# Performance work log

Hardware: AMD Instinct MI355X
Metric: run time of the kernel (lower is better)

## Reference

```python
import jax, jax.numpy as jnp
import numpy as np

H = 1024           # hidden_dim
BS = 32            # batch size
STEPS = 128        # number of chart steps
AMB = 32           # ambiguous decompositions per cell (padded fixed)
START = 256        # start_index: number of pre-filled leaf entries
CHART_LEN = START + STEPS


def setup_inputs() -> dict:
    key = jax.random.key(0)
    k1, k2, k3, k4 = jax.random.split(key, 4)
    chart = jax.random.normal(k1, (BS, CHART_LEN, 2 * H), dtype=jnp.float32)
    # (l, r) child positions per step/batch/ambiguity; valid filled entries in [0, START)
    operations = jax.random.randint(k2, (STEPS, BS, AMB, 2), 0, START, dtype=jnp.int32)
    U = jax.random.uniform(k3, (5 * H, 2 * H), dtype=jnp.float32)
    b = jnp.zeros((5 * H,), dtype=jnp.float32)
    energy_u = jax.random.uniform(k4, (H,), dtype=jnp.float32)
    return {"chart": chart, "operations": operations, "start_index": START,
            "U": U, "b": b, "energy_u": energy_u}


def reference(chart, operations, start_index, U, b, energy_u):
    h_dim = energy_u.shape[0]
    bs, amb = chart.shape[0], operations.shape[2]
    batch_idx = jnp.arange(bs)[:, None, None]  # [bs,1,1] for gather broadcast
    temperature = jnp.float32(1.0)
    eps = jnp.float32(1e-8)  # torch cosine_similarity eps
    u_norm = jnp.maximum(jnp.linalg.norm(energy_u), eps)

    def step_fn(ch, inp):
        step, ops = inp  # ops: [bs, amb, 2]
        # gather child chart entries: [bs, amb, 2, 2H]
        entries = ch[batch_idx, ops, :]
        ccL = entries[:, :, 0, :h_dim]                 # left cell state  [bs,amb,H]
        ccR = entries[:, :, 1, :h_dim]                 # right cell state [bs,amb,H]
        hh = entries[:, :, :, h_dim:].reshape(bs, amb, 2 * h_dim)  # [hL;hR]
        preact = jnp.einsum('bah,gh->bag', hh, U) + b  # [bs,amb,5H]
        i  = jax.nn.sigmoid(preact[..., :h_dim])
        fL = jax.nn.sigmoid(preact[..., h_dim:2 * h_dim])
        fR = jax.nn.sigmoid(preact[..., 2 * h_dim:3 * h_dim])
        o  = jax.nn.sigmoid(preact[..., 3 * h_dim:4 * h_dim])
        u  = jnp.tanh(preact[..., 4 * h_dim:])
        c = fL * ccL + fR * ccR + i * u                # [bs,amb,H]
        h = o * jnp.tanh(c)                            # [bs,amb,H]
        # cosine-similarity energy against learned vector energy_u
        h_norm = jnp.maximum(jnp.linalg.norm(h, axis=2), eps)  # [bs,amb]
        e = (h @ energy_u) / (u_norm * h_norm)                 # [bs,amb]
        s = jax.nn.softmax(e / temperature, axis=1)[..., None] # [bs,amb,1]
        combined = jnp.concatenate([(s * c).sum(axis=1), (s * h).sum(axis=1)], axis=-1)
        ch = ch.at[:, start_index + step, :].set(combined)
        return ch, None

    n_steps = operations.shape[0]
    chart, _ = jax.lax.scan(step_fn, chart, (jnp.arange(n_steps), operations))
    return chart
```

## Files before the change

### kernel.cpp

```cpp
#include <hip/hip_runtime.h>
#include <hip/hip_fp16.h>


typedef unsigned int u32;
typedef unsigned short u16;
typedef __attribute__((ext_vector_type(8))) short short8;
typedef __attribute__((ext_vector_type(4))) float f32x4;
typedef __attribute__((ext_vector_type(4))) u16 u16x4;
typedef _Float16 h8 __attribute__((ext_vector_type(8)));
typedef _Float16 h2v __attribute__((ext_vector_type(2)));
typedef _Float16 h4v __attribute__((ext_vector_type(4)));

#define CHART_ROWS 384
#define L2E 1.4426950408889634f

__device__ __forceinline__ u16 f2bf(float f) {
  u32 u = __float_as_uint(f);
  u32 r = u + 0x7fffu + ((u >> 16) & 1u);
  return (u16)(r >> 16);
}

__device__ __forceinline__ h2v pk_exp2(h2v x) {
  __half2 t = *(__half2*)&x;
  t = h2exp2(t);
  return *(h2v*)&t;
}
__device__ __forceinline__ h2v pk_rcp(h2v x) {
  __half2 t = *(__half2*)&x;
  t = h2rcp(t);
  return *(h2v*)&t;
}

#if __has_builtin(__builtin_amdgcn_fdot2)
__device__ __forceinline__ float fdot2a(h2v a, h2v b, float c) {
  return __builtin_amdgcn_fdot2(a, b, c, false);
}
#else
__device__ __forceinline__ float fdot2a(h2v a, h2v b, float c) {
  return c + (float)a[0] * (float)b[0] + (float)a[1] * (float)b[1];
}
#endif

__device__ __forceinline__ void async16(const void* g, void* l) {
  __builtin_amdgcn_global_load_lds((const __attribute__((address_space(1))) u32*)g,
                                   (__attribute__((address_space(3))) u32*)l, 16, 0, 0);
}

#define BAR() __builtin_amdgcn_s_barrier()
#define VMCNT4 asm volatile("s_waitcnt vmcnt(4)" ::: "memory")
#define VMCNT0 asm volatile("s_waitcnt vmcnt(0)" ::: "memory")

__global__ void k_cvt(const f32x4* __restrict__ U4, u16* __restrict__ Ubf,
                      const float* __restrict__ chart, u16* __restrict__ chb,
                      _Float16* __restrict__ chc, float* __restrict__ out) {
  if (blockIdx.x < 10240) {
    int i = blockIdx.x * 256 + threadIdx.x;
    int row = i >> 9;
    float sc = (row < 4096) ? -L2E : (2.0f * L2E);
    f32x4 v = U4[i];
    u16x4 o = {f2bf(v[0] * sc), f2bf(v[1] * sc), f2bf(v[2] * sc), f2bf(v[3] * sc)};
    *(u16x4*)(Ubf + (size_t)i * 4) = o;
  } else {
    int i = (blockIdx.x - 10240) * 256 + threadIdx.x;
    int row = i >> 8;
    int k4 = (i & 255) * 4;
    int b = row >> 8, op = row & 255;
    const size_t base = (size_t)(b * CHART_ROWS + op) * 2048;
    const f32x4 vh = *(const f32x4*)(chart + base + 1024 + k4);
    const f32x4 vc = *(const f32x4*)(chart + base + k4);
    u16x4 oh = {f2bf(vh[0]), f2bf(vh[1]), f2bf(vh[2]), f2bf(vh[3])};
    h4v oc = {(_Float16)vc[0], (_Float16)vc[1], (_Float16)vc[2], (_Float16)vc[3]};
    *(u16x4*)(chb + (size_t)row * 1024 + k4) = oh;
    *(h4v*)(chc + (size_t)row * 1024 + k4) = oc;
    __builtin_nontemporal_store(vc, (f32x4*)(out + base + k4));
    __builtin_nontemporal_store(vh, (f32x4*)(out + base + 1024 + k4));
  }
}

#define LOAD_A(BUFO, MH) do { \
  _Pragma("unroll") \
  for (int i_ = 0; i_ < 4; ++i_) { \
    a[0][i_] = *(const short8*)(As + (BUFO) + am + (MH)*4096 + i_*1024 + sl0); \
    a[1][i_] = *(const short8*)(As + (BUFO) + am + (MH)*4096 + i_*1024 + sl1); \
  } } while (0)

#define LOAD_B(BUFO, NH, BR) do { \
  _Pragma("unroll") \
  for (int j_ = 0; j_ < 2; ++j_) { \
    BR[0][j_] = *(const short8*)(Bs + (BUFO) + bm + (NH)*2048 + j_*1024 + sl0); \
    BR[1][j_] = *(const short8*)(Bs + (BUFO) + bm + (NH)*2048 + j_*1024 + sl1); \
  } } while (0)

#define MFMA_Q(MH, NH, BR) do { \
  __builtin_amdgcn_s_setprio(1); \
  _Pragma("unroll") \
  for (int kk_ = 0; kk_ < 2; ++kk_) \
    _Pragma("unroll") \
    for (int i_ = 0; i_ < 4; ++i_) \
      _Pragma("unroll") \
      for (int j_ = 0; j_ < 2; ++j_) \
        acc[(MH)*4+i_][(NH)*2+j_] = __builtin_amdgcn_mfma_f32_16x16x32_bf16( \
            a[kk_][i_], BR[kk_][j_], acc[(MH)*4+i_][(NH)*2+j_], 0, 0, 0); \
  __builtin_amdgcn_s_setprio(0); } while (0)

__global__ __launch_bounds__(512, 2) void k_gemm_p(
    const u16* __restrict__ chb, const u16* __restrict__ Ubf,
    const float* __restrict__ bias, _Float16* __restrict__ P, int bgh_base)
{
  __shared__ u16 As[2 * 256 * 64];
  __shared__ u16 Bs[2 * 256 * 64];

  const int tid = threadIdx.x;
  const int wid = tid >> 6, lane = tid & 63;
  const int lane15 = lane & 15, quad = lane >> 4;
  const int wr = wid >> 2, wc = wid & 3;

  const int nwg = gridDim.x * gridDim.y;
  const int flat = blockIdx.y * gridDim.x + blockIdx.x;
  const int swz = (flat & 7) * (nwg >> 3) + (flat >> 3);
  const int bx = swz % 20;
  const int by = swz / 20;
  const int bghl = by >> 3;
  const int bgh = bgh_base + bghl;
  const int bg = bgh >> 1, uhalf = bgh & 1;
  const int mtile = by & 7;

  const u16* aSrc[2]; const u16* bSrc[2]; int dOff[2];
#pragma unroll
  for (int rnd = 0; rnd < 2; ++rnd) {
    int idx = rnd * 512 + tid;
    int r = idx >> 3, s = idx & 7, c = s ^ (r & 7);
    aSrc[rnd] = chb + (size_t)(bg * 2048 + mtile * 256 + r) * 1024 + c * 8;
    bSrc[rnd] = Ubf + (size_t)(bx * 256 + r) * 2048 + uhalf * 1024 + c * 8;
    dOff[rnd] = idx * 8;
  }
  auto STAGE_A = [&](int buf, int h, int T) {
#pragma unroll
    for (int rnd = 0; rnd < 2; ++rnd)
      async16(aSrc[rnd] + (size_t)h * 131072 + T * 64,
              As + buf * 16384 + h * 8192 + dOff[rnd]);
  };
  auto STAGE_B = [&](int buf, int h, int T) {
#pragma unroll
    for (int rnd = 0; rnd < 2; ++rnd)
      async16(bSrc[rnd] + (size_t)h * 262144 + T * 64,
              Bs + buf * 16384 + h * 8192 + dOff[rnd]);
  };

  const int sl0 = ((0 * 4 + quad) ^ (lane15 & 7)) * 8;
  const int sl1 = ((1 * 4 + quad) ^ (lane15 & 7)) * 8;
  const int am = (wr * 128 + lane15) * 64;
  const int bm = (wc * 64 + lane15) * 64;

  f32x4 acc[8][4];
#pragma unroll
  for (int m_ = 0; m_ < 8; ++m_)
#pragma unroll
    for (int n_ = 0; n_ < 4; ++n_) acc[m_][n_] = (f32x4){0.f, 0.f, 0.f, 0.f};

  short8 a[2][4], b0[2][2], b1[2][2];

  STAGE_B(0, 0, 0); STAGE_B(0, 1, 0); STAGE_A(0, 0, 0); STAGE_A(0, 1, 0);
  STAGE_B(1, 0, 1); STAGE_B(1, 1, 1);
  VMCNT4;
  BAR();

  for (int it = 0; it < 8; ++it) {
    const int T1 = 2 * it + 1, T2 = 2 * it + 2, T3 = 2 * it + 3;
    const bool e2 = (T2 < 16), e3 = (T3 < 16);
    LOAD_A(0, 0); LOAD_B(0, 0, b0);
    STAGE_A(1, 0, T1);
    BAR(); MFMA_Q(0, 0, b0); BAR();

    LOAD_B(0, 1, b1);
    STAGE_A(1, 1, T1);
    BAR(); MFMA_Q(0, 1, b1); BAR();

    LOAD_A(0, 1);
    if (e2) STAGE_B(0, 0, T2);
    BAR(); MFMA_Q(1, 0, b0); BAR();

    if (e2) STAGE_B(0, 1, T2);
    BAR(); MFMA_Q(1, 1, b1);
    if (e2) { VMCNT4; } else { VMCNT0; }
    BAR();
    LOAD_A(16384, 0); LOAD_B(16384, 0, b0);
    if (e2) STAGE_A(0, 0, T2);
    BAR(); MFMA_Q(0, 0, b0); BAR();

    LOAD_B(16384, 1, b1);
    if (e2) STAGE_A(0, 1, T2);
    BAR(); MFMA_Q(0, 1, b1); BAR();

    LOAD_A(16384, 1);
    if (e3) STAGE_B(1, 0, T3);
    BAR(); MFMA_Q(1, 0, b0); BAR();

    if (e3) STAGE_B(1, 1, T3);
    BAR(); MFMA_Q(1, 1, b1);
    if (e3) { VMCNT4; }
    BAR();
  }

  float bb[4];
#pragma unroll
  for (int nt = 0; nt < 4; ++nt) {
    int g = bx * 256 + wc * 64 + nt * 16 + lane15;
    float sc = (g < 4096) ? -L2E : (2.0f * L2E);
    bb[nt] = (uhalf == 0) ? bias[g] * sc : 0.f;
  }
  _Float16* Pb = P + ((size_t)bghl * 2048 + mtile * 256 + wr * 128) * 5120
               + bx * 256 + wc * 64;
#pragma unroll
  for (int mt = 0; mt < 8; ++mt)
#pragma unroll
    for (int rg = 0; rg < 4; ++rg) {
      _Float16* pr = Pb + (size_t)(mt * 16 + quad * 4 + rg) * 5120;
#pragma unroll
      for (int nt = 0; nt < 4; ++nt)
        __builtin_nontemporal_store((_Float16)(acc[mt][nt][rg] + bb[nt]),
                                    pr + nt * 16 + lane15);
    }
}

__global__ __launch_bounds__(256, 2) void k_fused(
    const _Float16* __restrict__ chc, const _Float16* __restrict__ P,
    const int* __restrict__ ops, const float* __restrict__ eu,
    float* __restrict__ out, int bg0)
{
  __shared__ float rS[4 * 2048];
  __shared__ float sS[4];

  const int tid = threadIdx.x;
  const int wave = tid >> 6, lane = tid & 63;
  const int flat = blockIdx.x;
  const int b_local = flat & 7;
  const int idx = flat >> 3;
  const int step = idx & 127;
  const int bgl = idx >> 7;
  const int b = (bg0 + bgl) * 8 + b_local;
  const size_t HSLAB = (size_t)2048 * 5120;
  const _Float16* Pl = P + (size_t)(2 * bgl) * HSLAB;

  float uf[2][8];
#pragma unroll
  for (int sub = 0; sub < 2; ++sub) {
    *(f32x4*)&uf[sub][0] = *(const f32x4*)(eu + sub * 512 + lane * 8);
    *(f32x4*)&uf[sub][4] = *(const f32x4*)(eu + sub * 512 + lane * 8 + 4);
  }
  float part = 0.f;
#pragma unroll
  for (int sub = 0; sub < 2; ++sub)
#pragma unroll
    for (int j = 0; j < 8; ++j) part += uf[sub][j] * uf[sub][j];
#pragma unroll
  for (int m = 1; m < 64; m <<= 1) part += __shfl_xor(part, m, 64);
  const float unorm = fmaxf(sqrtf(part), 1e-8f);
  h2v uu2[2][4];
#pragma unroll
  for (int sub = 0; sub < 2; ++sub)
#pragma unroll
    for (int p = 0; p < 4; ++p)
      uu2[sub][p] = (h2v){(_Float16)uf[sub][2 * p], (_Float16)uf[sub][2 * p + 1]};

  const h2v one2 = {(_Float16)1.0f, (_Float16)1.0f};
  const h2v m2h  = {(_Float16)(-2.0f), (_Float16)(-2.0f)};
  const h2v k2c  = {(_Float16)(2.0f * L2E), (_Float16)(2.0f * L2E)};

  float Sc[2][8], Sh[2][8];
#pragma unroll
  for (int sub = 0; sub < 2; ++sub)
#pragma unroll
    for (int j = 0; j < 8; ++j) { Sc[sub][j] = 0.f; Sh[sub][j] = 0.f; }
  float Ssum = 0.f;

  for (int rr = 0; rr < 8; ++rr) {
    const int a = wave * 8 + rr;
    const long opflat = (((long)step * 32 + b) * 32 + a) * 2;
    const int opL = ops[opflat], opR = ops[opflat + 1];
    const _Float16* PLp = Pl + (size_t)(b_local * 256 + opL) * 5120;
    const _Float16* PRp = Pl + HSLAB + (size_t)(b_local * 256 + opR) * 5120;
    const _Float16* ccL = chc + (size_t)(b * 256 + opL) * 1024;
    const _Float16* ccR = chc + (size_t)(b * 256 + opR) * 1024;
    float dot = 0.f, nn = 0.f;
    h2v cv[2][4], hv[2][4];
#pragma unroll
    for (int sub = 0; sub < 2; ++sub) {
      const int cb = sub * 512 + lane * 8;
      h2v pr2[5][4];
#pragma unroll
      for (int q = 0; q < 5; ++q) {
        h8 t8 = *(const h8*)(PLp + q * 1024 + cb) + *(const h8*)(PRp + q * 1024 + cb);
        *(h8*)&pr2[q][0] = t8;
      }
      h2v cl2[4], cr2[4];
      *(h8*)&cl2[0] = *(const h8*)(ccL + cb);
      *(h8*)&cr2[0] = *(const h8*)(ccR + cb);
#pragma unroll
      for (int p = 0; p < 4; ++p) {
        h2v sI = pk_rcp(one2 + pk_exp2(pr2[0][p]));
        h2v sL = pk_rcp(one2 + pk_exp2(pr2[1][p]));
        h2v sR = pk_rcp(one2 + pk_exp2(pr2[2][p]));
        h2v sO = pk_rcp(one2 + pk_exp2(pr2[3][p]));
        h2v rU = pk_rcp(one2 + pk_exp2(pr2[4][p]));
        h2v tU = one2 + m2h * rU;
        h2v c2 = sL * cl2[p] + sR * cr2[p] + sI * tU;
        h2v rC = pk_rcp(one2 + pk_exp2(c2 * k2c));
        h2v tC = one2 + m2h * rC;
        h2v hx = sO * tC;
        cv[sub][p] = c2; hv[sub][p] = hx;
        dot = fdot2a(hx, uu2[sub][p], dot);
        nn  = fdot2a(hx, hx, nn);
      }
    }
#pragma unroll
    for (int m = 1; m < 64; m <<= 1) {
      dot += __shfl_xor(dot, m, 64);
      nn  += __shfl_xor(nn, m, 64);
    }
    const float e = dot / (unorm * fmaxf(sqrtf(nn), 1e-8f));
    const float w = __builtin_amdgcn_exp2f(e * L2E);
    Ssum += w;
#pragma unroll
    for (int sub = 0; sub < 2; ++sub)
#pragma unroll
      for (int p = 0; p < 4; ++p) {
        Sc[sub][2 * p]     += w * (float)cv[sub][p][0];
        Sc[sub][2 * p + 1] += w * (float)cv[sub][p][1];
        Sh[sub][2 * p]     += w * (float)hv[sub][p][0];
        Sh[sub][2 * p + 1] += w * (float)hv[sub][p][1];
      }
  }

  if (lane == 0) sS[wave] = Ssum;
#pragma unroll
  for (int sub = 0; sub < 2; ++sub) {
    const int cb = sub * 512 + lane * 8;
    *(f32x4*)&rS[wave * 2048 + cb]            = *(f32x4*)&Sc[sub][0];
    *(f32x4*)&rS[wave * 2048 + cb + 4]        = *(f32x4*)&Sc[sub][4];
    *(f32x4*)&rS[wave * 2048 + 1024 + cb]     = *(f32x4*)&Sh[sub][0];
    *(f32x4*)&rS[wave * 2048 + 1024 + cb + 4] = *(f32x4*)&Sh[sub][4];
  }
  __syncthreads();

  const float inv = 1.0f / (sS[0] + sS[1] + sS[2] + sS[3]);
  float* orow = out + ((size_t)b * CHART_ROWS + 256 + step) * 2048;
#pragma unroll
  for (int half = 0; half < 2; ++half) {
#pragma unroll
    for (int sub = 0; sub < 2; ++sub) {
      const int cb = sub * 512 + lane * 8;
      const int off = half * 1024 + cb;
      float s0 = 0.f, s1 = 0.f, s2 = 0.f, s3 = 0.f;
      float s4 = 0.f, s5 = 0.f, s6 = 0.f, s7 = 0.f;
#pragma unroll
      for (int w8 = 0; w8 < 4; ++w8) {
        const f32x4 v0 = *(const f32x4*)&rS[w8 * 2048 + off];
        const f32x4 v1 = *(const f32x4*)&rS[w8 * 2048 + off + 4];
        s0 += v0[0]; s1 += v0[1]; s2 += v0[2]; s3 += v0[3];
        s4 += v1[0]; s5 += v1[1]; s6 += v1[2]; s7 += v1[3];
      }
      __builtin_nontemporal_store(
          (f32x4){s0 * inv, s1 * inv, s2 * inv, s3 * inv}, (f32x4*)(orow + off));
      __builtin_nontemporal_store(
          (f32x4){s4 * inv, s5 * inv, s6 * inv, s7 * inv}, (f32x4*)(orow + off + 4));
    }
  }
}

extern "C" void kernel_launch(void* const* d_in, const int* in_sizes, int n_in,
                              void* d_out, int out_size, void* d_ws, size_t ws_size,
                              hipStream_t stream) {
  (void)in_sizes; (void)n_in; (void)out_size;
  const float* chart = (const float*)d_in[0];
  const int*   ops   = (const int*)d_in[1];
  const float* U     = (const float*)d_in[3];
  const float* bias  = (const float*)d_in[4];
  const float* eu    = (const float*)d_in[5];
  float* out = (float*)d_out;
  char* ws = (char*)d_ws;

  u16*      Ubf = (u16*)ws;
  u16*      chb = (u16*)(ws + 20971520);
  _Float16* chc = (_Float16*)(ws + 37748736);
  _Float16* P   = (_Float16*)(ws + 54525952);
  const size_t SLAB = (size_t)2048 * 5120;
  const bool big = ws_size >= (size_t)54525952 + 8 * SLAB * 2;

  k_cvt<<<18432, 256, 0, stream>>>((const f32x4*)U, Ubf, chart, chb, chc, out);

  if (big) {
    k_gemm_p<<<dim3(20, 64), 512, 0, stream>>>(chb, Ubf, bias, P, 0);
    k_fused<<<4096, 256, 0, stream>>>(chc, P, ops, eu, out, 0);
  } else {
    for (int bg = 0; bg < 4; ++bg) {
      k_gemm_p<<<dim3(20, 16), 512, 0, stream>>>(chb, Ubf, bias, P, 2 * bg);
      k_fused<<<1024, 256, 0, stream>>>(chc, P, ops, eu, out, bg);
    }
  }
}
```

Measured before the change: 602.2 us.

## Split fused cell loop into two half-passes staging first-half cells in LDS

```diff
diff --git a/kernel.cpp b/kernel.cpp
--- a/kernel.cpp
+++ b/kernel.cpp
@@ -218,8 +218,7 @@
       _Float16* pr = Pb + (size_t)(mt * 16 + quad * 4 + rg) * 5120;
 #pragma unroll
       for (int nt = 0; nt < 4; ++nt)
-        __builtin_nontemporal_store((_Float16)(acc[mt][nt][rg] + bb[nt]),
-                                    pr + nt * 16 + lane15);
+        pr[nt * 16 + lane15] = (_Float16)(acc[mt][nt][rg] + bb[nt]);
     }
 }
 
@@ -241,6 +240,7 @@
   const int b = (bg0 + bgl) * 8 + b_local;
   const size_t HSLAB = (size_t)2048 * 5120;
   const _Float16* Pl = P + (size_t)(2 * bgl) * HSLAB;
+  _Float16* cP = (_Float16*)rS + wave * 4096;
 
   float uf[2][8];
 #pragma unroll
@@ -273,45 +273,81 @@
 #pragma unroll
     for (int j = 0; j < 8; ++j) { Sc[sub][j] = 0.f; Sh[sub][j] = 0.f; }
   float Ssum = 0.f;
+
+  h2v hP[8][4];
+  float dotP[8], nnP[8];
 
   for (int rr = 0; rr < 8; ++rr) {
     const int a = wave * 8 + rr;
     const long opflat = (((long)step * 32 + b) * 32 + a) * 2;
     const int opL = ops[opflat], opR = ops[opflat + 1];
-    const _Float16* PLp = Pl + (size_t)(b_local * 256 + opL) * 5120;
-    const _Float16* PRp = Pl + HSLAB + (size_t)(b_local * 256 + opR) * 5120;
-    const _Float16* ccL = chc + (size_t)(b * 256 + opL) * 1024;
-    const _Float16* ccR = chc + (size_t)(b * 256 + opR) * 1024;
+    const int cb = lane * 8;
+    const _Float16* PLp = Pl + (size_t)(b_local * 256 + opL) * 5120 + cb;
+    const _Float16* PRp = Pl + HSLAB + (size_t)(b_local * 256 + opR) * 5120 + cb;
+    h2v pr2[5][4];
+#pragma unroll
+    for (int q = 0; q < 5; ++q) {
+      h8 t8 = *(const h8*)(PLp + q * 1024) + *(const h8*)(PRp + q * 1024);
+      *(h8*)&pr2[q][0] = t8;
+    }
+    h2v cl2[4], cr2[4];
+    *(h8*)&cl2[0] = *(const h8*)(chc + (size_t)(b * 256 + opL) * 1024 + cb);
+    *(h8*)&cr2[0] = *(const h8*)(chc + (size_t)(b * 256 + opR) * 1024 + cb);
     float dot = 0.f, nn = 0.f;
-    h2v cv[2][4], hv[2][4];
-#pragma unroll
-    for (int sub = 0; sub < 2; ++sub) {
-      const int cb = sub * 512 + lane * 8;
-      h2v pr2[5][4];
-#pragma unroll
-      for (int q = 0; q < 5; ++q) {
-        h8 t8 = *(const h8*)(PLp + q * 1024 + cb) + *(const h8*)(PRp + q * 1024 + cb);
-        *(h8*)&pr2[q][0] = t8;
-      }
-      h2v cl2[4], cr2[4];
-      *(h8*)&cl2[0] = *(const h8*)(ccL + cb);
-      *(h8*)&cr2[0] = *(const h8*)(ccR + cb);
-#pragma unroll
-      for (int p = 0; p < 4; ++p) {
-        h2v sI = pk_rcp(one2 + pk_exp2(pr2[0][p]));
-        h2v sL = pk_rcp(one2 + pk_exp2(pr2[1][p]));
-        h2v sR = pk_rcp(one2 + pk_exp2(pr2[2][p]));
-        h2v sO = pk_rcp(one2 + pk_exp2(pr2[3][p]));
-        h2v rU = pk_rcp(one2 + pk_exp2(pr2[4][p]));
-        h2v tU = one2 + m2h * rU;
-        h2v c2 = sL * cl2[p] + sR * cr2[p] + sI * tU;
-        h2v rC = pk_rcp(one2 + pk_exp2(c2 * k2c));
-        h2v tC = one2 + m2h * rC;
-        h2v hx = sO * tC;
-        cv[sub][p] = c2; hv[sub][p] = hx;
-        dot = fdot2a(hx, uu2[sub][p], dot);
-        nn  = fdot2a(hx, hx, nn);
-      }
+    h2v cv4[4];
+#pragma unroll
+    for (int p = 0; p < 4; ++p) {
+      h2v sI = pk_rcp(one2 + pk_exp2(pr2[0][p]));
+      h2v sL = pk_rcp(one2 + pk_exp2(pr2[1][p]));
+      h2v sR = pk_rcp(one2 + pk_exp2(pr2[2][p]));
+      h2v sO = pk_rcp(one2 + pk_exp2(pr2[3][p]));
+      h2v rU = pk_rcp(one2 + pk_exp2(pr2[4][p]));
+      h2v tU = one2 + m2h * rU;
+      h2v c2 = sL * cl2[p] + sR * cr2[p] + sI * tU;
+      h2v rC = pk_rcp(one2 + pk_exp2(c2 * k2c));
+      h2v tC = one2 + m2h * rC;
+      h2v hx = sO * tC;
+      cv4[p] = c2; hP[rr][p] = hx;
+      dot = fdot2a(hx, uu2[0][p], dot);
+      nn  = fdot2a(hx, hx, nn);
+    }
+    *(h8*)(cP + rr * 512 + lane * 8) = *(h8*)&cv4[0];
+    dotP[rr] = dot; nnP[rr] = nn;
+  }
+
+  for (int rr = 0; rr < 8; ++rr) {
+    const int a = wave * 8 + rr;
+    const long opflat = (((long)step * 32 + b) * 32 + a) * 2;
+    const int opL = ops[opflat], opR = ops[opflat + 1];
+    const int cb = 512 + lane * 8;
+    const _Float16* PLp = Pl + (size_t)(b_local * 256 + opL) * 5120 + cb;
+    const _Float16* PRp = Pl + HSLAB + (size_t)(b_local * 256 + opR) * 5120 + cb;
+    h2v pr2[5][4];
+#pragma unroll
+    for (int q = 0; q < 5; ++q) {
+      h8 t8 = *(const h8*)(PLp + q * 1024) + *(const h8*)(PRp + q * 1024);
+      *(h8*)&pr2[q][0] = t8;
+    }
+    h2v cl2[4], cr2[4];
+    *(h8*)&cl2[0] = *(const h8*)(chc + (size_t)(b * 256 + opL) * 1024 + cb);
+    *(h8*)&cr2[0] = *(const h8*)(chc + (size_t)(b * 256 + opR) * 1024 + cb);
+    float dot = dotP[rr], nn = nnP[rr];
+    h2v cv1[4], hv1[4];
+#pragma unroll
+    for (int p = 0; p < 4; ++p) {
+      h2v sI = pk_rcp(one2 + pk_exp2(pr2[0][p]));
+      h2v sL = pk_rcp(one2 + pk_exp2(pr2[1][p]));
+      h2v sR = pk_rcp(one2 + pk_exp2(pr2[2][p]));
+      h2v sO = pk_rcp(one2 + pk_exp2(pr2[3][p]));
+      h2v rU = pk_rcp(one2 + pk_exp2(pr2[4][p]));
+      h2v tU = one2 + m2h * rU;
+      h2v c2 = sL * cl2[p] + sR * cr2[p] + sI * tU;
+      h2v rC = pk_rcp(one2 + pk_exp2(c2 * k2c));
+      h2v tC = one2 + m2h * rC;
+      h2v hx = sO * tC;
+      cv1[p] = c2; hv1[p] = hx;
+      dot = fdot2a(hx, uu2[1][p], dot);
+      nn  = fdot2a(hx, hx, nn);
     }
 #pragma unroll
     for (int m = 1; m < 64; m <<= 1) {
@@ -321,15 +357,19 @@
     const float e = dot / (unorm * fmaxf(sqrtf(nn), 1e-8f));
     const float w = __builtin_amdgcn_exp2f(e * L2E);
     Ssum += w;
-#pragma unroll
-    for (int sub = 0; sub < 2; ++sub)
-#pragma unroll
-      for (int p = 0; p < 4; ++p) {
-        Sc[sub][2 * p]     += w * (float)cv[sub][p][0];
-        Sc[sub][2 * p + 1] += w * (float)cv[sub][p][1];
-        Sh[sub][2 * p]     += w * (float)hv[sub][p][0];
-        Sh[sub][2 * p + 1] += w * (float)hv[sub][p][1];
-      }
+    h2v cp4[4];
+    *(h8*)&cp4[0] = *(const h8*)(cP + rr * 512 + lane * 8);
+#pragma unroll
+    for (int p = 0; p < 4; ++p) {
+      Sc[1][2 * p]     += w * (float)cv1[p][0];
+      Sc[1][2 * p + 1] += w * (float)cv1[p][1];
+      Sh[1][2 * p]     += w * (float)hv1[p][0];
+      Sh[1][2 * p + 1] += w * (float)hv1[p][1];
+      Sc[0][2 * p]     += w * (float)cp4[p][0];
+      Sc[0][2 * p + 1] += w * (float)cp4[p][1];
+      Sh[0][2 * p]     += w * (float)hP[rr][p][0];
+      Sh[0][2 * p + 1] += w * (float)hP[rr][p][1];
+    }
   }
 
   if (lane == 0) sS[wave] = Ssum;
```

Measured after the change: 1.407 ms. 134% more time.
